# Performance work log

Measured on AMD Instinct MI355X. Metric: run time of the kernel, lower is better.

The kernel has to match this reference:

```python
import jax, jax.numpy as jnp
import numpy as np

N = 50000
E = 1600000
D_IN, D_H1, D_H2 = 256, 128, 64


def setup_inputs() -> dict:
    key = jax.random.key(0)
    ks = jax.random.split(key, 16)
    def lin(k, fan_in, fan_out):
        # torch nn.Linear default init: U(-1/sqrt(fan_in), 1/sqrt(fan_in))
        kw, kb = jax.random.split(k)
        bound = 1.0 / np.sqrt(fan_in)
        W = jax.random.uniform(kw, (fan_out, fan_in), jnp.float32, -bound, bound)
        b = jax.random.uniform(kb, (fan_out,), jnp.float32, -bound, bound)
        return W, b
    x = jax.random.normal(ks[0], (N, D_IN), jnp.float32)
    edge_index = jax.random.randint(ks[1], (2, E), 0, N, jnp.int64)
    edge_weight = jax.random.uniform(ks[2], (E,), jnp.float32)
    enc1_w, enc1_b = lin(ks[3], D_IN, D_H1)
    enc2_w, enc2_b = lin(ks[4], D_H1, D_H2)
    gcn1_w, gcn1_b = lin(ks[5], D_H2, D_H2)
    gcn2_w, gcn2_b = lin(ks[6], D_H2, D_H2)
    dec1_w, dec1_b = lin(ks[7], D_H2, D_H1)
    dec2_w, dec2_b = lin(ks[8], D_H1, D_IN)
    return dict(x=x, edge_index=edge_index, edge_weight=edge_weight,
                enc1_w=enc1_w, enc1_b=enc1_b, enc2_w=enc2_w, enc2_b=enc2_b,
                gcn1_w=gcn1_w, gcn1_b=gcn1_b, gcn2_w=gcn2_w, gcn2_b=gcn2_b,
                dec1_w=dec1_w, dec1_b=dec1_b, dec2_w=dec2_w, dec2_b=dec2_b)


def _gcn_conv(h, src, dst, w_all, W, b, n_nodes):
    # PyG GCNConv: h' = D^{-1/2}(A+I)D^{-1/2} (h W^T) + b; self-loops already in src/dst/w_all
    h = h @ W.T
    deg = jax.ops.segment_sum(w_all, dst, num_segments=n_nodes)
    dinv = jnp.where(deg > 0, jax.lax.rsqrt(jnp.maximum(deg, 1e-12)), 0.0)
    norm = dinv[src] * w_all * dinv[dst]                 # [E+N]
    msg = h[src] * norm[:, None]                         # gather + scale
    out = jax.ops.segment_sum(msg, dst, num_segments=n_nodes)  # scatter-add
    return out + b


def reference(x, edge_index, edge_weight,
              enc1_w, enc1_b, enc2_w, enc2_b,
              gcn1_w, gcn1_b, gcn2_w, gcn2_b,
              dec1_w, dec1_b, dec2_w, dec2_b):
    n = x.shape[0]
    # add self-loops (weight 1.0), as PyG GCNConv does by default
    loop = jnp.arange(n, dtype=edge_index.dtype)
    src = jnp.concatenate([edge_index[0], loop])
    dst = jnp.concatenate([edge_index[1], loop])
    w_all = jnp.concatenate([edge_weight, jnp.ones((n,), edge_weight.dtype)])

    h = jax.nn.relu(x @ enc1_w.T + enc1_b)
    h = jax.nn.relu(h @ enc2_w.T + enc2_b)
    h = jax.nn.relu(_gcn_conv(h, src, dst, w_all, gcn1_w, gcn1_b, n))
    h = jax.nn.relu(_gcn_conv(h, src, dst, w_all, gcn2_w, gcn2_b, n))
    h = jax.nn.relu(h @ dec1_w.T + dec1_b)
    h = h @ dec2_w.T + dec2_b
    return jax.nn.sigmoid(h)
```

## Files before the change

### kernel.cpp

```cpp
#include <hip/hip_runtime.h>


constexpr int NBLK = 128;
constexpr int GRP  = NBLK / 8;

typedef __attribute__((ext_vector_type(8))) short bf16x8;
typedef __attribute__((ext_vector_type(4))) float f32x4;

__device__ inline void split2(float f0, float f1, unsigned& hp, unsigned& lp) {
    unsigned u0 = __float_as_uint(f0), u1 = __float_as_uint(f1);
    hp = (u1 & 0xFFFF0000u) | (u0 >> 16);
    float r0 = f0 - __uint_as_float(u0 & 0xFFFF0000u);
    float r1 = f1 - __uint_as_float(u1 & 0xFFFF0000u);
    lp = (__float_as_uint(r1) & 0xFFFF0000u) | (__float_as_uint(r0) >> 16);
}

struct Bf16Pair { bf16x8 h, l; };
__device__ inline Bf16Pair split8(float4 a, float4 b) {
    union { unsigned u[4]; bf16x8 v; } H, L;
    split2(a.x, a.y, H.u[0], L.u[0]);
    split2(a.z, a.w, H.u[1], L.u[1]);
    split2(b.x, b.y, H.u[2], L.u[2]);
    split2(b.z, b.w, H.u[3], L.u[3]);
    Bf16Pair p; p.h = H.v; p.l = L.v; return p;
}

struct WSplitArgs {
    const float* src[6];
    unsigned short* hi[6];
    unsigned short* lo[6];
    int n[6];
};
__global__ __launch_bounds__(256) void split_w(WSplitArgs a) {
    const int L = blockIdx.y;
    const int i = blockIdx.x * 256 + threadIdx.x;
    if (i < a.n[L]) {
        float f = a.src[L][i];
        unsigned u = __float_as_uint(f);
        float r = f - __uint_as_float(u & 0xFFFF0000u);
        a.hi[L][i] = (unsigned short)(u >> 16);
        a.lo[L][i] = (unsigned short)(__float_as_uint(r) >> 16);
    }
}

template <int K, int M, int ACT, bool BIAS>
__global__ __launch_bounds__(256) void gemm_sp(const float* __restrict__ A,
                                               const unsigned short* __restrict__ Whp,
                                               const unsigned short* __restrict__ Wlp,
                                               const float* __restrict__ bias,
                                               float* __restrict__ C, int N) {
    static_assert(K % 64 == 0, "K%64");
    constexpr int KS = 64;
    __shared__ __align__(16) unsigned short Ah[64][72];
    __shared__ __align__(16) unsigned short Al[64][72];

    const int gx  = gridDim.x;
    const int nwg = gx * gridDim.y;
    {
    }
    const int o    = blockIdx.y * gx + blockIdx.x;
    const int xcd  = o & 7;
    const int idx  = o >> 3;
    const int q    = nwg >> 3, rr = nwg & 7;
    const int wgid = (xcd < rr ? xcd * (q + 1) : rr * (q + 1) + (xcd - rr) * q) + idx;
    const int foff     = (wgid % gx) * 64;
    const int nodeBase = (wgid / gx) * 64;

    const int tid  = threadIdx.x;
    const int lane = tid & 63;
    const int wid  = tid >> 6;
    const int wm   = wid >> 1;
    const int wn   = wid & 1;
    const int fr   = lane & 15;
    const int fg   = lane >> 4;

    const int srow = tid >> 2;
    const int sc0  = (tid & 3) * 16;
    int grow = nodeBase + srow;
    if (grow >= N) grow = N - 1;
    const float* aptr = A + (size_t)grow * K + sc0;

    float4 av[4];
#pragma unroll
    for (int i = 0; i < 4; ++i) av[i] = *(const float4*)(aptr + i * 4);

    f32x4 acc[2][2];
#pragma unroll
    for (int mf = 0; mf < 2; ++mf)
#pragma unroll
        for (int nf = 0; nf < 2; ++nf) acc[mf][nf] = (f32x4)0.f;

    for (int kc = 0; kc < K; kc += KS) {
        {
            Bf16Pair p0 = split8(av[0], av[1]);
            Bf16Pair p1 = split8(av[2], av[3]);
            *(bf16x8*)&Ah[srow][sc0]     = p0.h;
            *(bf16x8*)&Ah[srow][sc0 + 8] = p1.h;
            *(bf16x8*)&Al[srow][sc0]     = p0.l;
            *(bf16x8*)&Al[srow][sc0 + 8] = p1.l;
        }
        __syncthreads();

        if (kc + KS < K) {
#pragma unroll
            for (int i = 0; i < 4; ++i)
                av[i] = *(const float4*)(aptr + kc + KS + i * 4);
        }

#pragma unroll
        for (int kf = 0; kf < 2; ++kf) {
            const int kcol = kf * 32 + fg * 8;
            bf16x8 ah[2], al[2], bh[2], bl[2];
#pragma unroll
            for (int mf = 0; mf < 2; ++mf) {
                const int r = wm * 32 + mf * 16 + fr;
                ah[mf] = *(const bf16x8*)&Ah[r][kcol];
                al[mf] = *(const bf16x8*)&Al[r][kcol];
            }
#pragma unroll
            for (int nf = 0; nf < 2; ++nf) {
                const size_t wo = (size_t)(foff + wn * 32 + nf * 16 + fr) * K
                                  + kc + kcol;
                bh[nf] = *(const bf16x8*)(Whp + wo);
                bl[nf] = *(const bf16x8*)(Wlp + wo);
            }
#pragma unroll
            for (int mf = 0; mf < 2; ++mf)
#pragma unroll
                for (int nf = 0; nf < 2; ++nf) {
                    acc[mf][nf] = __builtin_amdgcn_mfma_f32_16x16x32_bf16(
                        ah[mf], bh[nf], acc[mf][nf], 0, 0, 0);
                    acc[mf][nf] = __builtin_amdgcn_mfma_f32_16x16x32_bf16(
                        al[mf], bh[nf], acc[mf][nf], 0, 0, 0);
                    acc[mf][nf] = __builtin_amdgcn_mfma_f32_16x16x32_bf16(
                        ah[mf], bl[nf], acc[mf][nf], 0, 0, 0);
                }
        }
        __syncthreads();
    }

#pragma unroll
    for (int nf = 0; nf < 2; ++nf) {
        const int feat = foff + wn * 32 + nf * 16 + fr;
        const float bv = BIAS ? bias[feat] : 0.f;
#pragma unroll
        for (int mf = 0; mf < 2; ++mf) {
            const int node0 = nodeBase + wm * 32 + mf * 16 + fg * 4;
#pragma unroll
            for (int i = 0; i < 4; ++i) {
                const int node = node0 + i;
                if (node < N) {
                    float x = acc[mf][nf][i] + bv;
                    if constexpr (ACT == 1) x = fmaxf(x, 0.f);
                    if constexpr (ACT == 2) x = 1.f / (1.f + __expf(-x));
                    C[(size_t)node * M + feat] = x;
                }
            }
        }
    }
}


__global__ __launch_bounds__(256) void count_k(const int* __restrict__ ei,
                                               int* __restrict__ cnt,
                                               int NB, int E) {
    __shared__ int hist[784];
    const int tid = threadIdx.x;
    for (int i = tid; i < NB; i += 256) hist[i] = 0;
    __syncthreads();
    const int chunk = (E + NBLK - 1) / NBLK;
    const int lo = blockIdx.x * chunk;
    const int hi = min(lo + chunk, E);
    for (int e = lo + tid; e < hi; e += 256) {
        int d = ei[E + e];
        atomicAdd(&hist[d >> 6], 1);
    }
    __syncthreads();
    const int r = blockIdx.x & 7, g = blockIdx.x >> 3;
    for (int i = tid; i < NB; i += 256)
        cnt[i * NBLK + r * GRP + g] = hist[i];
}

__global__ __launch_bounds__(256) void scan1(const int* __restrict__ cnt,
                                             int* __restrict__ pos,
                                             int* __restrict__ bs, int n) {
    __shared__ int s[256];
    const int t = threadIdx.x;
    const int i0 = blockIdx.x * 512 + 2 * t;
    int c0 = (i0     < n) ? cnt[i0]     : 0;
    int c1 = (i0 + 1 < n) ? cnt[i0 + 1] : 0;
    int c = c0 + c1;
    s[t] = c;
    __syncthreads();
    for (int off = 1; off < 256; off <<= 1) {
        int v = (t >= off) ? s[t - off] : 0;
        __syncthreads();
        s[t] += v;
        __syncthreads();
    }
    int excl = s[t] - c;
    if (i0     < n) pos[i0]     = excl;
    if (i0 + 1 < n) pos[i0 + 1] = excl + c0;
    if (t == 255) bs[blockIdx.x] = s[255];
}

__global__ __launch_bounds__(256) void scan_tops(int* __restrict__ bs, int nb) {
    __shared__ int s[256];
    int t = threadIdx.x;
    int v = (t < nb) ? bs[t] : 0;
    s[t] = v;
    __syncthreads();
    for (int off = 1; off < 256; off <<= 1) {
        int u = (t >= off) ? s[t - off] : 0;
        __syncthreads();
        s[t] += u;
        __syncthreads();
    }
    if (t < nb) bs[t] = s[t] - v;
}

__global__ __launch_bounds__(256) void scan2(int* __restrict__ pos,
                                             const int* __restrict__ bs,
                                             int* __restrict__ bucketBase,
                                             int n, int NB, int E) {
    const int t = threadIdx.x;
    const int i0 = blockIdx.x * 512 + 2 * t;
    const int add = bs[blockIdx.x];
#pragma unroll
    for (int c = 0; c < 2; ++c) {
        int i = i0 + c;
        if (i < n) {
            int v = pos[i] + add;
            pos[i] = v;
            if ((i & (NBLK - 1)) == 0) bucketBase[i >> 7] = v;
        }
    }
    if (blockIdx.x == 0 && t == 0) bucketBase[NB] = E;
}

__global__ __launch_bounds__(256) void place_k(const int* __restrict__ ei,
                                               const float* __restrict__ w,
                                               const int* __restrict__ pos,
                                               int2* __restrict__ ebuf,
                                               int NB, int E) {
    __shared__ int cur[784];
    const int tid = threadIdx.x;
    const int r = blockIdx.x & 7, g = blockIdx.x >> 3;
    for (int i = tid; i < NB; i += 256) cur[i] = pos[i * NBLK + r * GRP + g];
    __syncthreads();
    const int chunk = (E + NBLK - 1) / NBLK;
    const int lo = blockIdx.x * chunk;
    const int hi = min(lo + chunk, E);
    for (int e = lo + tid; e < hi; e += 256) {
        int s = ei[e];
        int d = ei[E + e];
        float wv = w[e];
        int p = atomicAdd(&cur[d >> 6], 1);
        ebuf[p] = make_int2(s | ((d & 63) << 26), __float_as_int(wv));
    }
}

__global__ __launch_bounds__(256) void bucket_build(const int2* __restrict__ ebuf,
                                                    const int* __restrict__ bucketBase,
                                                    int2* __restrict__ sn,
                                                    int* __restrict__ row,
                                                    float* __restrict__ dinv,
                                                    int N, int E) {
    __shared__ int   lh[64];
    __shared__ float ldg[64];
    __shared__ int   sc[64];
    __shared__ int   lofs[64];
    const int tid  = threadIdx.x;
    const int base = bucketBase[blockIdx.x];
    const int end  = bucketBase[blockIdx.x + 1];

    if (tid < 64) { lh[tid] = 0; ldg[tid] = 0.f; }
    __syncthreads();
    for (int i = base + tid; i < end; i += 256) {
        int2 v = ebuf[i];
        int dl = ((unsigned)v.x) >> 26;
        atomicAdd(&lh[dl], 1);
        atomicAdd(&ldg[dl], __int_as_float(v.y));
    }
    __syncthreads();
    if (tid < 64) sc[tid] = lh[tid];
    __syncthreads();
    for (int off = 1; off < 64; off <<= 1) {
        int v = (tid < 64 && tid >= off) ? sc[tid - off] : 0;
        __syncthreads();
        if (tid < 64) sc[tid] += v;
        __syncthreads();
    }
    if (tid < 64) {
        int excl = sc[tid] - lh[tid];
        int d = (blockIdx.x << 6) + tid;
        if (d < N) {
            row[d]  = base + excl;
            dinv[d] = rsqrtf(fmaxf(1.0f + ldg[tid], 1e-12f));
        }
        lofs[tid] = base + excl;
    }
    __syncthreads();
    for (int i = base + tid; i < end; i += 256) {
        int2 v = ebuf[i];
        unsigned u = (unsigned)v.x;
        int dl = u >> 26;
        int s  = u & 0x03FFFFFF;
        int p  = atomicAdd(&lofs[dl], 1);
        sn[p] = make_int2(s, v.y);
    }
    if (blockIdx.x == 0 && tid == 0) row[N] = E;
}

__global__ __launch_bounds__(256) void scale_pay(int2* __restrict__ sn,
                                                 const float* __restrict__ dinv,
                                                 int E) {
    int p = blockIdx.x * 256 + threadIdx.x;
    if (p < E) {
        int2 v = sn[p];
        sn[p] = make_int2(v.x, __float_as_int(__int_as_float(v.y) * dinv[v.x]));
    }
}

__global__ __launch_bounds__(256) void gcn_agg(const float* __restrict__ t,
                                               const int2* __restrict__ sn,
                                               const int* __restrict__ row,
                                               const float* __restrict__ dinv,
                                               const float* __restrict__ bias,
                                               float* __restrict__ out, int N) {
    const int lane = threadIdx.x & 63;
    int i = __builtin_amdgcn_readfirstlane((int)(blockIdx.x * 4) + (threadIdx.x >> 6));
    if (i >= N) return;
    float di   = dinv[i];
    float self = t[(size_t)i * 64 + lane];
    float acc  = 0.f;
    int p  = row[i];
    int pe = row[i + 1];
    for (; p + 4 <= pe; p += 4) {
        int2 v0 = sn[p];
        int2 v1 = sn[p + 1];
        int2 v2 = sn[p + 2];
        int2 v3 = sn[p + 3];
        acc += t[(size_t)v0.x * 64 + lane] * __int_as_float(v0.y);
        acc += t[(size_t)v1.x * 64 + lane] * __int_as_float(v1.y);
        acc += t[(size_t)v2.x * 64 + lane] * __int_as_float(v2.y);
        acc += t[(size_t)v3.x * 64 + lane] * __int_as_float(v3.y);
    }
    for (; p < pe; ++p) {
        int2 v = sn[p];
        acc += t[(size_t)v.x * 64 + lane] * __int_as_float(v.y);
    }
    float x = (acc + self * di) * di + bias[lane];
    out[(size_t)i * 64 + lane] = fmaxf(x, 0.f);
}

extern "C" void kernel_launch(void* const* d_in, const int* in_sizes, int n_in,
                              void* d_out, int out_size, void* d_ws, size_t ws_size,
                              hipStream_t stream) {
    const float* x      = (const float*)d_in[0];
    const int*   ei     = (const int*)d_in[1];
    const float* ew     = (const float*)d_in[2];
    const float* enc1_w = (const float*)d_in[3];
    const float* enc1_b = (const float*)d_in[4];
    const float* enc2_w = (const float*)d_in[5];
    const float* enc2_b = (const float*)d_in[6];
    const float* gcn1_w = (const float*)d_in[7];
    const float* gcn1_b = (const float*)d_in[8];
    const float* gcn2_w = (const float*)d_in[9];
    const float* gcn2_b = (const float*)d_in[10];
    const float* dec1_w = (const float*)d_in[11];
    const float* dec1_b = (const float*)d_in[12];
    const float* dec2_w = (const float*)d_in[13];
    const float* dec2_b = (const float*)d_in[14];

    const int N  = in_sizes[0] / 256;
    const int E  = in_sizes[2];
    const int NB = (N + 63) / 64;
    const int NCNT = NB * NBLK;
    const int NS   = (NCNT + 511) / 512;

    float* ws   = (float*)d_ws;
    float* bufA = ws;
    int2*  sn   = (int2*)bufA;
    float* bufC = bufA + (size_t)2 * E;
    int2*  ebuf = (int2*)bufC;
    float* bufB = bufA + (size_t)N * 128;
    float* dinv = bufB + (size_t)N * 64;
    int*   row  = (int*)(dinv + N);
    int*   cnt  = row + (N + 1);
    int*   pos  = cnt + NCNT;
    int*   bucketBase = pos + NCNT;
    int*   bs   = bucketBase + (NB + 1);
    unsigned short* whi = (unsigned short*)(bs + 256);
    unsigned short* wlo = whi + 90112;

    const int nodeTiles = (N + 63) / 64;
    const int nBlkE     = (E + 255) / 256;

    WSplitArgs wa;
    const float* wsrc[6] = {enc1_w, enc2_w, gcn1_w, gcn2_w, dec1_w, dec2_w};
    const int    wsz[6]  = {32768, 8192, 4096, 4096, 8192, 32768};
    const int    woff[6] = {0, 32768, 40960, 45056, 49152, 57344};
    for (int l = 0; l < 6; ++l) {
        wa.src[l] = wsrc[l];
        wa.hi[l]  = whi + woff[l];
        wa.lo[l]  = wlo + woff[l];
        wa.n[l]   = wsz[l];
    }
    split_w<<<dim3(128, 6), 256, 0, stream>>>(wa);

    gemm_sp<256, 128, 1, true><<<dim3(2, nodeTiles), 256, 0, stream>>>(
        x, whi + woff[0], wlo + woff[0], enc1_b, bufA, N);
    gemm_sp<128, 64, 1, true><<<dim3(1, nodeTiles), 256, 0, stream>>>(
        bufA, whi + woff[1], wlo + woff[1], enc2_b, bufB, N);

    count_k<<<NBLK, 256, 0, stream>>>(ei, cnt, NB, E);
    scan1<<<NS, 256, 0, stream>>>(cnt, pos, bs, NCNT);
    scan_tops<<<1, 256, 0, stream>>>(bs, NS);
    scan2<<<NS, 256, 0, stream>>>(pos, bs, bucketBase, NCNT, NB, E);
    place_k<<<NBLK, 256, 0, stream>>>(ei, ew, pos, ebuf, NB, E);
    bucket_build<<<NB, 256, 0, stream>>>(ebuf, bucketBase, sn, row, dinv, N, E);
    scale_pay<<<nBlkE, 256, 0, stream>>>(sn, dinv, E);

    gemm_sp<64, 64, 0, false><<<dim3(1, nodeTiles), 256, 0, stream>>>(
        bufB, whi + woff[2], wlo + woff[2], nullptr, bufC, N);
    gcn_agg<<<(N + 3) / 4, 256, 0, stream>>>(bufC, sn, row, dinv, gcn1_b, bufB, N);

    gemm_sp<64, 64, 0, false><<<dim3(1, nodeTiles), 256, 0, stream>>>(
        bufB, whi + woff[3], wlo + woff[3], nullptr, bufC, N);
    gcn_agg<<<(N + 3) / 4, 256, 0, stream>>>(bufC, sn, row, dinv, gcn2_b, bufB, N);

    gemm_sp<64, 128, 1, true><<<dim3(2, nodeTiles), 256, 0, stream>>>(
        bufB, whi + woff[4], wlo + woff[4], dec1_b, bufA, N);
    gemm_sp<128, 256, 2, true><<<dim3(4, nodeTiles), 256, 0, stream>>>(
        bufA, whi + woff[5], wlo + woff[5], dec2_b, (float*)d_out, N);
}
```

Measured before the change: 458.9 us.

## Compute all output feature tiles per block in GEMMs and widen aggregation unroll

Each GEMM block now covers the full output width (FT feature tiles) for its 64-node tile. The input rows are loaded and bf16-split into shared memory once instead of once per feature tile, and the XCD-aware block remapping is dropped. In exchange, register pressure rises with FT*4 accumulators (64 floats per thread for dec2), and the grid has fewer blocks, which may lower occupancy and parallelism. Separately, the GCN aggregation loop is unrolled by 8 with a partial sum to get more gathers in flight.

```diff
diff --git a/kernel.cpp b/kernel.cpp
--- a/kernel.cpp
+++ b/kernel.cpp
@@ -43,36 +43,26 @@
     }
 }
 
-template <int K, int M, int ACT, bool BIAS>
-__global__ __launch_bounds__(256) void gemm_sp(const float* __restrict__ A,
+template <int K, int M, int FT, int ACT, bool BIAS>
+__global__ __launch_bounds__(256) void gemm_ft(const float* __restrict__ A,
                                                const unsigned short* __restrict__ Whp,
                                                const unsigned short* __restrict__ Wlp,
                                                const float* __restrict__ bias,
                                                float* __restrict__ C, int N) {
     static_assert(K % 64 == 0, "K%64");
+    static_assert(FT * 64 == M, "FT*64==M");
     constexpr int KS = 64;
     __shared__ __align__(16) unsigned short Ah[64][72];
     __shared__ __align__(16) unsigned short Al[64][72];
 
-    const int gx  = gridDim.x;
-    const int nwg = gx * gridDim.y;
-    {
-    }
-    const int o    = blockIdx.y * gx + blockIdx.x;
-    const int xcd  = o & 7;
-    const int idx  = o >> 3;
-    const int q    = nwg >> 3, rr = nwg & 7;
-    const int wgid = (xcd < rr ? xcd * (q + 1) : rr * (q + 1) + (xcd - rr) * q) + idx;
-    const int foff     = (wgid % gx) * 64;
-    const int nodeBase = (wgid / gx) * 64;
-
-    const int tid  = threadIdx.x;
-    const int lane = tid & 63;
-    const int wid  = tid >> 6;
-    const int wm   = wid >> 1;
-    const int wn   = wid & 1;
-    const int fr   = lane & 15;
-    const int fg   = lane >> 4;
+    const int tid      = threadIdx.x;
+    const int lane     = tid & 63;
+    const int wid      = tid >> 6;
+    const int wm       = wid >> 1;
+    const int wn       = wid & 1;
+    const int fr       = lane & 15;
+    const int fg       = lane >> 4;
+    const int nodeBase = blockIdx.x * 64;
 
     const int srow = tid >> 2;
     const int sc0  = (tid & 3) * 16;
@@ -84,11 +74,13 @@
 #pragma unroll
     for (int i = 0; i < 4; ++i) av[i] = *(const float4*)(aptr + i * 4);
 
-    f32x4 acc[2][2];
-#pragma unroll
-    for (int mf = 0; mf < 2; ++mf)
-#pragma unroll
-        for (int nf = 0; nf < 2; ++nf) acc[mf][nf] = (f32x4)0.f;
+    f32x4 acc[FT][2][2];
+#pragma unroll
+    for (int ft = 0; ft < FT; ++ft)
+#pragma unroll
+        for (int mf = 0; mf < 2; ++mf)
+#pragma unroll
+            for (int nf = 0; nf < 2; ++nf) acc[ft][mf][nf] = (f32x4)0.f;
 
     for (int kc = 0; kc < K; kc += KS) {
         {
@@ -110,7 +102,7 @@
 #pragma unroll
         for (int kf = 0; kf < 2; ++kf) {
             const int kcol = kf * 32 + fg * 8;
-            bf16x8 ah[2], al[2], bh[2], bl[2];
+            bf16x8 ah[2], al[2];
 #pragma unroll
             for (int mf = 0; mf < 2; ++mf) {
                 const int r = wm * 32 + mf * 16 + fr;
@@ -118,30 +110,36 @@
                 al[mf] = *(const bf16x8*)&Al[r][kcol];
             }
 #pragma unroll
-            for (int nf = 0; nf < 2; ++nf) {
-                const size_t wo = (size_t)(foff + wn * 32 + nf * 16 + fr) * K
-                                  + kc + kcol;
-                bh[nf] = *(const bf16x8*)(Whp + wo);
-                bl[nf] = *(const bf16x8*)(Wlp + wo);
+            for (int ft = 0; ft < FT; ++ft) {
+                bf16x8 bh[2], bl[2];
+#pragma unroll
+                for (int nf = 0; nf < 2; ++nf) {
+                    const size_t wo =
+                        (size_t)(ft * 64 + wn * 32 + nf * 16 + fr) * K + kc + kcol;
+                    bh[nf] = *(const bf16x8*)(Whp + wo);
+                    bl[nf] = *(const bf16x8*)(Wlp + wo);
+                }
+#pragma unroll
+                for (int mf = 0; mf < 2; ++mf)
+#pragma unroll
+                    for (int nf = 0; nf < 2; ++nf) {
+                        acc[ft][mf][nf] = __builtin_amdgcn_mfma_f32_16x16x32_bf16(
+                            ah[mf], bh[nf], acc[ft][mf][nf], 0, 0, 0);
+                        acc[ft][mf][nf] = __builtin_amdgcn_mfma_f32_16x16x32_bf16(
+                            al[mf], bh[nf], acc[ft][mf][nf], 0, 0, 0);
+                        acc[ft][mf][nf] = __builtin_amdgcn_mfma_f32_16x16x32_bf16(
+                            ah[mf], bl[nf], acc[ft][mf][nf], 0, 0, 0);
+                    }
             }
-#pragma unroll
-            for (int mf = 0; mf < 2; ++mf)
-#pragma unroll
-                for (int nf = 0; nf < 2; ++nf) {
-                    acc[mf][nf] = __builtin_amdgcn_mfma_f32_16x16x32_bf16(
-                        ah[mf], bh[nf], acc[mf][nf], 0, 0, 0);
-                    acc[mf][nf] = __builtin_amdgcn_mfma_f32_16x16x32_bf16(
-                        al[mf], bh[nf], acc[mf][nf], 0, 0, 0);
-                    acc[mf][nf] = __builtin_amdgcn_mfma_f32_16x16x32_bf16(
-                        ah[mf], bl[nf], acc[mf][nf], 0, 0, 0);
-                }
-        }
-        __syncthreads();
-    }
-
+        }
+        __syncthreads();
+    }
+
+#pragma unroll
+    for (int ft = 0; ft < FT; ++ft)
 #pragma unroll
     for (int nf = 0; nf < 2; ++nf) {
-        const int feat = foff + wn * 32 + nf * 16 + fr;
+        const int feat = ft * 64 + wn * 32 + nf * 16 + fr;
         const float bv = BIAS ? bias[feat] : 0.f;
 #pragma unroll
         for (int mf = 0; mf < 2; ++mf) {
@@ -150,7 +148,7 @@
             for (int i = 0; i < 4; ++i) {
                 const int node = node0 + i;
                 if (node < N) {
-                    float x = acc[mf][nf][i] + bv;
+                    float x = acc[ft][mf][nf][i] + bv;
                     if constexpr (ACT == 1) x = fmaxf(x, 0.f);
                     if constexpr (ACT == 2) x = 1.f / (1.f + __expf(-x));
                     C[(size_t)node * M + feat] = x;
@@ -336,15 +334,15 @@
     float acc  = 0.f;
     int p  = row[i];
     int pe = row[i + 1];
-    for (; p + 4 <= pe; p += 4) {
-        int2 v0 = sn[p];
-        int2 v1 = sn[p + 1];
-        int2 v2 = sn[p + 2];
-        int2 v3 = sn[p + 3];
-        acc += t[(size_t)v0.x * 64 + lane] * __int_as_float(v0.y);
-        acc += t[(size_t)v1.x * 64 + lane] * __int_as_float(v1.y);
-        acc += t[(size_t)v2.x * 64 + lane] * __int_as_float(v2.y);
-        acc += t[(size_t)v3.x * 64 + lane] * __int_as_float(v3.y);
+    for (; p + 8 <= pe; p += 8) {
+        int2 v[8];
+#pragma unroll
+        for (int j = 0; j < 8; ++j) v[j] = sn[p + j];
+        float partial = 0.f;
+#pragma unroll
+        for (int j = 0; j < 8; ++j)
+            partial += t[(size_t)v[j].x * 64 + lane] * __int_as_float(v[j].y);
+        acc += partial;
     }
     for (; p < pe; ++p) {
         int2 v = sn[p];
@@ -409,9 +407,9 @@
     }
     split_w<<<dim3(128, 6), 256, 0, stream>>>(wa);
 
-    gemm_sp<256, 128, 1, true><<<dim3(2, nodeTiles), 256, 0, stream>>>(
+    gemm_ft<256, 128, 2, 1, true><<<nodeTiles, 256, 0, stream>>>(
         x, whi + woff[0], wlo + woff[0], enc1_b, bufA, N);
-    gemm_sp<128, 64, 1, true><<<dim3(1, nodeTiles), 256, 0, stream>>>(
+    gemm_ft<128, 64, 1, 1, true><<<nodeTiles, 256, 0, stream>>>(
         bufA, whi + woff[1], wlo + woff[1], enc2_b, bufB, N);
 
     count_k<<<NBLK, 256, 0, stream>>>(ei, cnt, NB, E);
@@ -422,16 +420,16 @@
     bucket_build<<<NB, 256, 0, stream>>>(ebuf, bucketBase, sn, row, dinv, N, E);
     scale_pay<<<nBlkE, 256, 0, stream>>>(sn, dinv, E);
 
-    gemm_sp<64, 64, 0, false><<<dim3(1, nodeTiles), 256, 0, stream>>>(
+    gemm_ft<64, 64, 1, 0, false><<<nodeTiles, 256, 0, stream>>>(
         bufB, whi + woff[2], wlo + woff[2], nullptr, bufC, N);
     gcn_agg<<<(N + 3) / 4, 256, 0, stream>>>(bufC, sn, row, dinv, gcn1_b, bufB, N);
 
-    gemm_sp<64, 64, 0, false><<<dim3(1, nodeTiles), 256, 0, stream>>>(
+    gemm_ft<64, 64, 1, 0, false><<<nodeTiles, 256, 0, stream>>>(
         bufB, whi + woff[3], wlo + woff[3], nullptr, bufC, N);
     gcn_agg<<<(N + 3) / 4, 256, 0, stream>>>(bufC, sn, row, dinv, gcn2_b, bufB, N);
 
-    gemm_sp<64, 128, 1, true><<<dim3(2, nodeTiles), 256, 0, stream>>>(
+    gemm_ft<64, 128, 2, 1, true><<<nodeTiles, 256, 0, stream>>>(
         bufB, whi + woff[4], wlo + woff[4], dec1_b, bufA, N);
-    gemm_sp<128, 256, 2, true><<<dim3(4, nodeTiles), 256, 0, stream>>>(
+    gemm_ft<128, 256, 4, 2, true><<<nodeTiles, 256, 0, stream>>>(
         bufA, whi + woff[5], wlo + woff[5], dec2_b, (float*)d_out, N);
 }
```

Measured after the change: 475.7 us. 1.04x slower.

## Make split-bf16 GEMM persistent over node tiles with cross-tile prefetch; widen aggregation unroll

Applied to the files above, without the earlier changes.

The GEMM kernel becomes semi-persistent. Each workgroup loops over several node tiles (half the tiles per feature column for the wider layers) and prefetches the next tile's A rows while the current tile's MFMAs run. This halves the block count for the multi-feature-tile GEMMs and amortises launch and prologue latency, though fewer blocks means less parallelism to hide latency. The GCN aggregation inner loop is also unrolled to 8 neighbours with a partial sum, to raise memory-level parallelism on the gathers.

```diff
diff --git a/kernel.cpp b/kernel.cpp
--- a/kernel.cpp
+++ b/kernel.cpp
@@ -43,28 +43,26 @@
     }
 }
 
-template <int K, int M, int ACT, bool BIAS>
-__global__ __launch_bounds__(256) void gemm_sp(const float* __restrict__ A,
+template <int K, int M, int FTC, int ACT, bool BIAS>
+__global__ __launch_bounds__(256) void gemm_ps(const float* __restrict__ A,
                                                const unsigned short* __restrict__ Whp,
                                                const unsigned short* __restrict__ Wlp,
                                                const float* __restrict__ bias,
-                                               float* __restrict__ C, int N) {
+                                               float* __restrict__ C, int N,
+                                               int nodeTiles, int bpf) {
     static_assert(K % 64 == 0, "K%64");
-    constexpr int KS = 64;
+    constexpr int KSTEPS = K / 64;
     __shared__ __align__(16) unsigned short Ah[64][72];
     __shared__ __align__(16) unsigned short Al[64][72];
 
-    const int gx  = gridDim.x;
-    const int nwg = gx * gridDim.y;
-    {
-    }
-    const int o    = blockIdx.y * gx + blockIdx.x;
-    const int xcd  = o & 7;
-    const int idx  = o >> 3;
-    const int q    = nwg >> 3, rr = nwg & 7;
+    const int nwg = gridDim.x;
+    const int o   = blockIdx.x;
+    const int xcd = o & 7, idx = o >> 3;
+    const int q   = nwg >> 3, rr = nwg & 7;
     const int wgid = (xcd < rr ? xcd * (q + 1) : rr * (q + 1) + (xcd - rr) * q) + idx;
-    const int foff     = (wgid % gx) * 64;
-    const int nodeBase = (wgid / gx) * 64;
+    const int ft   = wgid % FTC;
+    const int foff = ft * 64;
+    const int t0   = wgid / FTC;
 
     const int tid  = threadIdx.x;
     const int lane = tid & 63;
@@ -76,84 +74,105 @@
 
     const int srow = tid >> 2;
     const int sc0  = (tid & 3) * 16;
-    int grow = nodeBase + srow;
-    if (grow >= N) grow = N - 1;
-    const float* aptr = A + (size_t)grow * K + sc0;
-
-    float4 av[4];
-#pragma unroll
-    for (int i = 0; i < 4; ++i) av[i] = *(const float4*)(aptr + i * 4);
-
-    f32x4 acc[2][2];
-#pragma unroll
-    for (int mf = 0; mf < 2; ++mf)
-#pragma unroll
-        for (int nf = 0; nf < 2; ++nf) acc[mf][nf] = (f32x4)0.f;
-
-    for (int kc = 0; kc < K; kc += KS) {
-        {
-            Bf16Pair p0 = split8(av[0], av[1]);
-            Bf16Pair p1 = split8(av[2], av[3]);
-            *(bf16x8*)&Ah[srow][sc0]     = p0.h;
-            *(bf16x8*)&Ah[srow][sc0 + 8] = p1.h;
-            *(bf16x8*)&Al[srow][sc0]     = p0.l;
-            *(bf16x8*)&Al[srow][sc0 + 8] = p1.l;
+
+    auto aPtr = [&](int tile) {
+        int grow = tile * 64 + srow;
+        if (grow >= N) grow = N - 1;
+        return A + (size_t)grow * K + sc0;
+    };
+
+    float4 av[4], av2[4];
+    if (t0 < nodeTiles) {
+        const float* p = aPtr(t0);
+#pragma unroll
+        for (int i = 0; i < 4; ++i) av[i] = *(const float4*)(p + i * 4);
+    }
+
+    for (int t = t0; t < nodeTiles; t += bpf) {
+        const float* apCur = aPtr(t);
+        f32x4 acc[2][2];
+#pragma unroll
+        for (int mf = 0; mf < 2; ++mf)
+#pragma unroll
+            for (int nf = 0; nf < 2; ++nf) acc[mf][nf] = (f32x4)0.f;
+
+#pragma unroll
+        for (int ks = 0; ks < KSTEPS; ++ks) {
+            const int kc = ks * 64;
+            {
+                Bf16Pair p0 = split8(av[0], av[1]);
+                Bf16Pair p1 = split8(av[2], av[3]);
+                *(bf16x8*)&Ah[srow][sc0]     = p0.h;
+                *(bf16x8*)&Ah[srow][sc0 + 8] = p1.h;
+                *(bf16x8*)&Al[srow][sc0]     = p0.l;
+                *(bf16x8*)&Al[srow][sc0 + 8] = p1.l;
+            }
+            __syncthreads();
+
+            {
+                const float* np = nullptr;
+                if (ks + 1 < KSTEPS) {
+                    np = apCur + kc + 64;
+                } else if (t + bpf < nodeTiles) {
+                    np = aPtr(t + bpf);
+                }
+                if (np) {
+#pragma unroll
+                    for (int i = 0; i < 4; ++i) av2[i] = *(const float4*)(np + i * 4);
+                }
+            }
+
+#pragma unroll
+            for (int kf = 0; kf < 2; ++kf) {
+                const int kcol = kf * 32 + fg * 8;
+                bf16x8 ah[2], al[2], bh[2], bl[2];
+#pragma unroll
+                for (int mf = 0; mf < 2; ++mf) {
+                    const int r = wm * 32 + mf * 16 + fr;
+                    ah[mf] = *(const bf16x8*)&Ah[r][kcol];
+                    al[mf] = *(const bf16x8*)&Al[r][kcol];
+                }
+#pragma unroll
+                for (int nf = 0; nf < 2; ++nf) {
+                    const size_t wo = (size_t)(foff + wn * 32 + nf * 16 + fr) * K
+                                      + kc + kcol;
+                    bh[nf] = *(const bf16x8*)(Whp + wo);
+                    bl[nf] = *(const bf16x8*)(Wlp + wo);
+                }
+#pragma unroll
+                for (int mf = 0; mf < 2; ++mf)
+#pragma unroll
+                    for (int nf = 0; nf < 2; ++nf) {
+                        acc[mf][nf] = __builtin_amdgcn_mfma_f32_16x16x32_bf16(
+                            ah[mf], bh[nf], acc[mf][nf], 0, 0, 0);
+                        acc[mf][nf] = __builtin_amdgcn_mfma_f32_16x16x32_bf16(
+                            al[mf], bh[nf], acc[mf][nf], 0, 0, 0);
+                        acc[mf][nf] = __builtin_amdgcn_mfma_f32_16x16x32_bf16(
+                            ah[mf], bl[nf], acc[mf][nf], 0, 0, 0);
+                    }
+            }
+            __syncthreads();
+#pragma unroll
+            for (int i = 0; i < 4; ++i) av[i] = av2[i];
         }
-        __syncthreads();
-
-        if (kc + KS < K) {
-#pragma unroll
-            for (int i = 0; i < 4; ++i)
-                av[i] = *(const float4*)(aptr + kc + KS + i * 4);
-        }
-
-#pragma unroll
-        for (int kf = 0; kf < 2; ++kf) {
-            const int kcol = kf * 32 + fg * 8;
-            bf16x8 ah[2], al[2], bh[2], bl[2];
+
+        const int nodeBase = t * 64;
+#pragma unroll
+        for (int nf = 0; nf < 2; ++nf) {
+            const int feat = foff + wn * 32 + nf * 16 + fr;
+            const float bv = BIAS ? bias[feat] : 0.f;
 #pragma unroll
             for (int mf = 0; mf < 2; ++mf) {
-                const int r = wm * 32 + mf * 16 + fr;
-                ah[mf] = *(const bf16x8*)&Ah[r][kcol];
-                al[mf] = *(const bf16x8*)&Al[r][kcol];
-            }
-#pragma unroll
-            for (int nf = 0; nf < 2; ++nf) {
-                const size_t wo = (size_t)(foff + wn * 32 + nf * 16 + fr) * K
-                                  + kc + kcol;
-                bh[nf] = *(const bf16x8*)(Whp + wo);
-                bl[nf] = *(const bf16x8*)(Wlp + wo);
-            }
-#pragma unroll
-            for (int mf = 0; mf < 2; ++mf)
-#pragma unroll
-                for (int nf = 0; nf < 2; ++nf) {
-                    acc[mf][nf] = __builtin_amdgcn_mfma_f32_16x16x32_bf16(
-                        ah[mf], bh[nf], acc[mf][nf], 0, 0, 0);
-                    acc[mf][nf] = __builtin_amdgcn_mfma_f32_16x16x32_bf16(
-                        al[mf], bh[nf], acc[mf][nf], 0, 0, 0);
-                    acc[mf][nf] = __builtin_amdgcn_mfma_f32_16x16x32_bf16(
-                        ah[mf], bl[nf], acc[mf][nf], 0, 0, 0);
-                }
-        }
-        __syncthreads();
-    }
-
-#pragma unroll
-    for (int nf = 0; nf < 2; ++nf) {
-        const int feat = foff + wn * 32 + nf * 16 + fr;
-        const float bv = BIAS ? bias[feat] : 0.f;
-#pragma unroll
-        for (int mf = 0; mf < 2; ++mf) {
-            const int node0 = nodeBase + wm * 32 + mf * 16 + fg * 4;
-#pragma unroll
-            for (int i = 0; i < 4; ++i) {
-                const int node = node0 + i;
-                if (node < N) {
-                    float x = acc[mf][nf][i] + bv;
-                    if constexpr (ACT == 1) x = fmaxf(x, 0.f);
-                    if constexpr (ACT == 2) x = 1.f / (1.f + __expf(-x));
-                    C[(size_t)node * M + feat] = x;
+                const int node0 = nodeBase + wm * 32 + mf * 16 + fg * 4;
+#pragma unroll
+                for (int i = 0; i < 4; ++i) {
+                    const int node = node0 + i;
+                    if (node < N) {
+                        float x = acc[mf][nf][i] + bv;
+                        if constexpr (ACT == 1) x = fmaxf(x, 0.f);
+                        if constexpr (ACT == 2) x = 1.f / (1.f + __expf(-x));
+                        C[(size_t)node * M + feat] = x;
+                    }
                 }
             }
         }
@@ -336,15 +355,15 @@
     float acc  = 0.f;
     int p  = row[i];
     int pe = row[i + 1];
-    for (; p + 4 <= pe; p += 4) {
-        int2 v0 = sn[p];
-        int2 v1 = sn[p + 1];
-        int2 v2 = sn[p + 2];
-        int2 v3 = sn[p + 3];
-        acc += t[(size_t)v0.x * 64 + lane] * __int_as_float(v0.y);
-        acc += t[(size_t)v1.x * 64 + lane] * __int_as_float(v1.y);
-        acc += t[(size_t)v2.x * 64 + lane] * __int_as_float(v2.y);
-        acc += t[(size_t)v3.x * 64 + lane] * __int_as_float(v3.y);
+    for (; p + 8 <= pe; p += 8) {
+        int2 v[8];
+#pragma unroll
+        for (int j = 0; j < 8; ++j) v[j] = sn[p + j];
+        float partial = 0.f;
+#pragma unroll
+        for (int j = 0; j < 8; ++j)
+            partial += t[(size_t)v[j].x * 64 + lane] * __int_as_float(v[j].y);
+        acc += partial;
     }
     for (; p < pe; ++p) {
         int2 v = sn[p];
@@ -395,6 +414,7 @@
     unsigned short* wlo = whi + 90112;
 
     const int nodeTiles = (N + 63) / 64;
+    const int halfTiles = (nodeTiles + 1) / 2;
     const int nBlkE     = (E + 255) / 256;
 
     WSplitArgs wa;
@@ -409,10 +429,10 @@
     }
     split_w<<<dim3(128, 6), 256, 0, stream>>>(wa);
 
-    gemm_sp<256, 128, 1, true><<<dim3(2, nodeTiles), 256, 0, stream>>>(
-        x, whi + woff[0], wlo + woff[0], enc1_b, bufA, N);
-    gemm_sp<128, 64, 1, true><<<dim3(1, nodeTiles), 256, 0, stream>>>(
-        bufA, whi + woff[1], wlo + woff[1], enc2_b, bufB, N);
+    gemm_ps<256, 128, 2, 1, true><<<2 * halfTiles, 256, 0, stream>>>(
+        x, whi + woff[0], wlo + woff[0], enc1_b, bufA, N, nodeTiles, halfTiles);
+    gemm_ps<128, 64, 1, 1, true><<<nodeTiles, 256, 0, stream>>>(
+        bufA, whi + woff[1], wlo + woff[1], enc2_b, bufB, N, nodeTiles, nodeTiles);
 
     count_k<<<NBLK, 256, 0, stream>>>(ei, cnt, NB, E);
     scan1<<<NS, 256, 0, stream>>>(cnt, pos, bs, NCNT);
@@ -422,16 +442,16 @@
     bucket_build<<<NB, 256, 0, stream>>>(ebuf, bucketBase, sn, row, dinv, N, E);
     scale_pay<<<nBlkE, 256, 0, stream>>>(sn, dinv, E);
 
-    gemm_sp<64, 64, 0, false><<<dim3(1, nodeTiles), 256, 0, stream>>>(
-        bufB, whi + woff[2], wlo + woff[2], nullptr, bufC, N);
+    gemm_ps<64, 64, 1, 0, false><<<nodeTiles, 256, 0, stream>>>(
+        bufB, whi + woff[2], wlo + woff[2], nullptr, bufC, N, nodeTiles, nodeTiles);
     gcn_agg<<<(N + 3) / 4, 256, 0, stream>>>(bufC, sn, row, dinv, gcn1_b, bufB, N);
 
-    gemm_sp<64, 64, 0, false><<<dim3(1, nodeTiles), 256, 0, stream>>>(
-        bufB, whi + woff[3], wlo + woff[3], nullptr, bufC, N);
+    gemm_ps<64, 64, 1, 0, false><<<nodeTiles, 256, 0, stream>>>(
+        bufB, whi + woff[3], wlo + woff[3], nullptr, bufC, N, nodeTiles, nodeTiles);
     gcn_agg<<<(N + 3) / 4, 256, 0, stream>>>(bufC, sn, row, dinv, gcn2_b, bufB, N);
 
-    gemm_sp<64, 128, 1, true><<<dim3(2, nodeTiles), 256, 0, stream>>>(
-        bufB, whi + woff[4], wlo + woff[4], dec1_b, bufA, N);
-    gemm_sp<128, 256, 2, true><<<dim3(4, nodeTiles), 256, 0, stream>>>(
-        bufA, whi + woff[5], wlo + woff[5], dec2_b, (float*)d_out, N);
-}
+    gemm_ps<64, 128, 2, 1, true><<<2 * halfTiles, 256, 0, stream>>>(
+        bufB, whi + woff[4], wlo + woff[4], dec1_b, bufA, N, nodeTiles, halfTiles);
+    gemm_ps<128, 256, 4, 2, true><<<4 * halfTiles, 256, 0, stream>>>(
+        bufA, whi + woff[5], wlo + woff[5], dec2_b, (float*)d_out, N, nodeTiles, halfTiles);
+}
```

Measured after the change: 443.9 us. -3.3%, faster.
